# Optimization experiments

Hardware: AMD Instinct MI355X
Metric: run time of the kernel (lower is better)

The kernel has to match this reference:

```python
import jax, jax.numpy as jnp
import numpy as np

B, T, F, H = 64, 128, 188, 16  # batch, time, in_features, feature_embed_dim
N_CONT = F - 11  # features 11.. are continuous (177)


def setup_inputs() -> dict:
    key = jax.random.key(0)
    ks = jax.random.split(key, 14)
    s = 1.0 / np.sqrt(H)  # nn.Linear default init scale
    u = lambda k, shape: jax.random.uniform(k, shape, jnp.float32, -s, s)
    return {
        "x": jax.random.normal(ks[0], (B, T, F * H), jnp.float32),
        # grouped per-feature Linear weights, grouped by output dim
        "W2a": u(ks[1], (4, H, 2)),  "b2a": u(ks[2], (4, 2)),   # features 0-3
        "W3":  u(ks[3], (2, H, 3)),  "b3":  u(ks[4], (2, 3)),   # features 4-5
        "W4":  u(ks[5], (1, H, 4)),  "b4":  u(ks[6], (1, 4)),   # feature 6
        "W6":  u(ks[7], (1, H, 6)),  "b6":  u(ks[8], (1, 6)),   # feature 7
        "W7":  u(ks[9], (3, H, 7)),  "b7":  u(ks[10], (3, 7)),  # features 8-10
        "Wc":  u(ks[11], (N_CONT, H, 2)), "bc": u(ks[12], (N_CONT, 2)),  # features 11..
        "eps": jax.random.normal(ks[13], (B * T, N_CONT), jnp.float32),  # normal-sampling noise
    }


def _cat_argmax(xg, W, b):
    # softmax then argmax == argmax of logits
    logits = jnp.einsum('nfd,fdo->nfo', xg, W) + b
    return jnp.argmax(logits, axis=-1).astype(jnp.float32)


def reference(x, W2a, b2a, W3, b3, W4, b4, W6, b6, W7, b7, Wc, bc, eps):
    xr = x.reshape(B * T, F, H)
    cats = jnp.concatenate([
        _cat_argmax(xr[:, 0:4],  W2a, b2a),
        _cat_argmax(xr[:, 4:6],  W3,  b3),
        _cat_argmax(xr[:, 6:7],  W4,  b4),
        _cat_argmax(xr[:, 7:8],  W6,  b6),
        _cat_argmax(xr[:, 8:11], W7,  b7),
    ], axis=1)  # [N, 11]
    dec = jnp.einsum('nfd,fdo->nfo', xr[:, 11:], Wc) + bc  # [N, 177, 2]
    mean = jnp.tanh(dec[..., 0])
    std = jax.nn.sigmoid(dec[..., 1])
    samp = mean + std * eps  # reparameterized t.normal(mean, std)
    outs = jnp.concatenate([cats, samp], axis=1)  # [N, 188]
    return outs.reshape(B, T, F)
```

## Files before the change

### kernel.cpp

```cpp
#include <hip/hip_runtime.h>
#include <hip/hip_bf16.h>
#include <cmath>

#define NROWS   8192
#define FDIM    188
#define HDIM    16
#define NCONT   177
#define NCAT    11
#define XSTRIDE 3008

__global__ __launch_bounds__(256)
void tab_cont_kernel(const float* __restrict__ x,
                     const float* __restrict__ Wc, const float* __restrict__ bc,
                     const float* __restrict__ eps,
                     float* __restrict__ out)
{
    const int t = blockIdx.x * blockDim.x + threadIdx.x;
    const int n  = t / NCONT;
    const int cf = t - n * NCONT;

    const float4* wp = reinterpret_cast<const float4*>(Wc + cf * 32);
    float4 w0 = wp[0], w1 = wp[1], w2 = wp[2], w3 = wp[3];
    float4 w4 = wp[4], w5 = wp[5], w6 = wp[6], w7 = wp[7];

    const float2 bb = reinterpret_cast<const float2*>(bc)[cf];
    const float  ev = eps[(size_t)n * NCONT + cf];

    const float4* xq = reinterpret_cast<const float4*>(
        x + (size_t)n * XSTRIDE + (size_t)(NCAT + cf) * HDIM);
    float4 a0 = xq[0], a1 = xq[1], a2 = xq[2], a3 = xq[3];

    float m = bb.x, s = bb.y;
    m = fmaf(a0.x, w0.x, m); s = fmaf(a0.x, w0.y, s);
    m = fmaf(a0.y, w0.z, m); s = fmaf(a0.y, w0.w, s);
    m = fmaf(a0.z, w1.x, m); s = fmaf(a0.z, w1.y, s);
    m = fmaf(a0.w, w1.z, m); s = fmaf(a0.w, w1.w, s);
    m = fmaf(a1.x, w2.x, m); s = fmaf(a1.x, w2.y, s);
    m = fmaf(a1.y, w2.z, m); s = fmaf(a1.y, w2.w, s);
    m = fmaf(a1.z, w3.x, m); s = fmaf(a1.z, w3.y, s);
    m = fmaf(a1.w, w3.z, m); s = fmaf(a1.w, w3.w, s);
    m = fmaf(a2.x, w4.x, m); s = fmaf(a2.x, w4.y, s);
    m = fmaf(a2.y, w4.z, m); s = fmaf(a2.y, w4.w, s);
    m = fmaf(a2.z, w5.x, m); s = fmaf(a2.z, w5.y, s);
    m = fmaf(a2.w, w5.z, m); s = fmaf(a2.w, w5.w, s);
    m = fmaf(a3.x, w6.x, m); s = fmaf(a3.x, w6.y, s);
    m = fmaf(a3.y, w6.z, m); s = fmaf(a3.y, w6.w, s);
    m = fmaf(a3.z, w7.x, m); s = fmaf(a3.z, w7.y, s);
    m = fmaf(a3.w, w7.z, m); s = fmaf(a3.w, w7.w, s);

    float mc   = fminf(fmaxf(m, -10.0f), 10.0f);
    float mean = 1.0f - 2.0f / (__expf(2.0f * mc) + 1.0f);
    float stdv = 1.0f / (1.0f + __expf(-s));

    out[(size_t)n * FDIM + NCAT + cf] = fmaf(stdv, ev, mean);
}

__global__ __launch_bounds__(256)
void tab_cat_kernel(const float* __restrict__ x,
                    const float* __restrict__ W2a, const float* __restrict__ b2a,
                    const float* __restrict__ W3,  const float* __restrict__ b3,
                    const float* __restrict__ W4,  const float* __restrict__ b4,
                    const float* __restrict__ W6,  const float* __restrict__ b6,
                    const float* __restrict__ W7,  const float* __restrict__ b7,
                    float* __restrict__ out)
{
    const int t = blockIdx.x * blockDim.x + threadIdx.x;
    if (t >= NROWS * NCAT) return;
    const int n = t / NCAT;
    const int f = t - n * NCAT;

    const float4* xq = reinterpret_cast<const float4*>(
        x + (size_t)n * XSTRIDE + (size_t)f * HDIM);
    float4 a0 = xq[0], a1 = xq[1], a2 = xq[2], a3 = xq[3];
    float xv[16] = { a0.x, a0.y, a0.z, a0.w,
                     a1.x, a1.y, a1.z, a1.w,
                     a2.x, a2.y, a2.z, a2.w,
                     a3.x, a3.y, a3.z, a3.w };

    const float *W, *bb;
    int odim;
    if (f < 4)      { W = W2a + f * HDIM * 2;      bb = b2a + f * 2;      odim = 2; }
    else if (f < 6) { W = W3 + (f - 4) * HDIM * 3; bb = b3 + (f - 4) * 3; odim = 3; }
    else if (f < 7) { W = W4;                      bb = b4;               odim = 4; }
    else if (f < 8) { W = W6;                      bb = b6;               odim = 6; }
    else            { W = W7 + (f - 8) * HDIM * 7; bb = b7 + (f - 8) * 7; odim = 7; }

    float best = -1e30f;
    int   bi   = 0;
    for (int o = 0; o < odim; ++o) {
        float acc = bb[o];
        #pragma unroll
        for (int d = 0; d < 16; ++d) acc = fmaf(xv[d], W[d * odim + o], acc);
        if (acc > best) { best = acc; bi = o; }
    }
    out[(size_t)n * FDIM + f] = (float)bi;
}

extern "C" void kernel_launch(void* const* d_in, const int* in_sizes, int n_in,
                              void* d_out, int out_size, void* d_ws, size_t ws_size,
                              hipStream_t stream) {
    const float* x   = (const float*)d_in[0];
    const float* W2a = (const float*)d_in[1];
    const float* b2a = (const float*)d_in[2];
    const float* W3  = (const float*)d_in[3];
    const float* b3  = (const float*)d_in[4];
    const float* W4  = (const float*)d_in[5];
    const float* b4  = (const float*)d_in[6];
    const float* W6  = (const float*)d_in[7];
    const float* b6  = (const float*)d_in[8];
    const float* W7  = (const float*)d_in[9];
    const float* b7  = (const float*)d_in[10];
    const float* Wc  = (const float*)d_in[11];
    const float* bc  = (const float*)d_in[12];
    const float* eps = (const float*)d_in[13];
    float* out = (float*)d_out;

    hipLaunchKernelGGL(tab_cont_kernel, dim3(NROWS * NCONT / 256), dim3(256), 0, stream,
                       x, Wc, bc, eps, out);
    hipLaunchKernelGGL(tab_cat_kernel, dim3(NROWS * NCAT / 256), dim3(256), 0, stream,
                       x, W2a, b2a, W3, b3, W4, b4, W6, b6, W7, b7, out);
}
```

Before: 190.4 us.

## Fuse continuous and categorical kernels into one launch with LDS-staged weights

Merges the two kernels into a single launch whose blocks branch on blockIdx into continuous or categorical work. Continuous blocks first stage all Wc weights and biases into shared memory in a transposed layout, then read them from LDS instead of global memory. This removes one launch and the gap between kernels. In exchange, every continuous block now pays a cooperative copy of about 23 KB of weights plus a barrier, and the LDS use may limit occupancy.

```diff
diff --git a/kernel.cpp b/kernel.cpp
--- a/kernel.cpp
+++ b/kernel.cpp
@@ -9,91 +9,106 @@
 #define NCAT    11
 #define XSTRIDE 3008
 
-__global__ __launch_bounds__(256)
-void tab_cont_kernel(const float* __restrict__ x,
-                     const float* __restrict__ Wc, const float* __restrict__ bc,
-                     const float* __restrict__ eps,
-                     float* __restrict__ out)
-{
-    const int t = blockIdx.x * blockDim.x + threadIdx.x;
-    const int n  = t / NCONT;
-    const int cf = t - n * NCONT;
+#define CONT_THREADS (NROWS * NCONT)
+#define CONT_BLOCKS  (CONT_THREADS / 256)
+#define CAT_THREADS  (NROWS * NCAT)
+#define CAT_BLOCKS   (CAT_THREADS / 256)
 
-    const float4* wp = reinterpret_cast<const float4*>(Wc + cf * 32);
-    float4 w0 = wp[0], w1 = wp[1], w2 = wp[2], w3 = wp[3];
-    float4 w4 = wp[4], w5 = wp[5], w6 = wp[6], w7 = wp[7];
-
-    const float2 bb = reinterpret_cast<const float2*>(bc)[cf];
-    const float  ev = eps[(size_t)n * NCONT + cf];
-
-    const float4* xq = reinterpret_cast<const float4*>(
-        x + (size_t)n * XSTRIDE + (size_t)(NCAT + cf) * HDIM);
-    float4 a0 = xq[0], a1 = xq[1], a2 = xq[2], a3 = xq[3];
-
-    float m = bb.x, s = bb.y;
-    m = fmaf(a0.x, w0.x, m); s = fmaf(a0.x, w0.y, s);
-    m = fmaf(a0.y, w0.z, m); s = fmaf(a0.y, w0.w, s);
-    m = fmaf(a0.z, w1.x, m); s = fmaf(a0.z, w1.y, s);
-    m = fmaf(a0.w, w1.z, m); s = fmaf(a0.w, w1.w, s);
-    m = fmaf(a1.x, w2.x, m); s = fmaf(a1.x, w2.y, s);
-    m = fmaf(a1.y, w2.z, m); s = fmaf(a1.y, w2.w, s);
-    m = fmaf(a1.z, w3.x, m); s = fmaf(a1.z, w3.y, s);
-    m = fmaf(a1.w, w3.z, m); s = fmaf(a1.w, w3.w, s);
-    m = fmaf(a2.x, w4.x, m); s = fmaf(a2.x, w4.y, s);
-    m = fmaf(a2.y, w4.z, m); s = fmaf(a2.y, w4.w, s);
-    m = fmaf(a2.z, w5.x, m); s = fmaf(a2.z, w5.y, s);
-    m = fmaf(a2.w, w5.z, m); s = fmaf(a2.w, w5.w, s);
-    m = fmaf(a3.x, w6.x, m); s = fmaf(a3.x, w6.y, s);
-    m = fmaf(a3.y, w6.z, m); s = fmaf(a3.y, w6.w, s);
-    m = fmaf(a3.z, w7.x, m); s = fmaf(a3.z, w7.y, s);
-    m = fmaf(a3.w, w7.z, m); s = fmaf(a3.w, w7.w, s);
-
-    float mc   = fminf(fmaxf(m, -10.0f), 10.0f);
-    float mean = 1.0f - 2.0f / (__expf(2.0f * mc) + 1.0f);
-    float stdv = 1.0f / (1.0f + __expf(-s));
-
-    out[(size_t)n * FDIM + NCAT + cf] = fmaf(stdv, ev, mean);
-}
 
 __global__ __launch_bounds__(256)
-void tab_cat_kernel(const float* __restrict__ x,
-                    const float* __restrict__ W2a, const float* __restrict__ b2a,
-                    const float* __restrict__ W3,  const float* __restrict__ b3,
-                    const float* __restrict__ W4,  const float* __restrict__ b4,
-                    const float* __restrict__ W6,  const float* __restrict__ b6,
-                    const float* __restrict__ W7,  const float* __restrict__ b7,
-                    float* __restrict__ out)
+void tab_fused_kernel(const float* __restrict__ x,
+                      const float* __restrict__ W2a, const float* __restrict__ b2a,
+                      const float* __restrict__ W3,  const float* __restrict__ b3,
+                      const float* __restrict__ W4,  const float* __restrict__ b4,
+                      const float* __restrict__ W6,  const float* __restrict__ b6,
+                      const float* __restrict__ W7,  const float* __restrict__ b7,
+                      const float* __restrict__ Wc,  const float* __restrict__ bc,
+                      const float* __restrict__ eps,
+                      float* __restrict__ out)
 {
-    const int t = blockIdx.x * blockDim.x + threadIdx.x;
-    if (t >= NROWS * NCAT) return;
-    const int n = t / NCAT;
-    const int f = t - n * NCAT;
+    __shared__ float4 sW[8 * NCONT];
+    __shared__ float2 sB[NCONT];
 
-    const float4* xq = reinterpret_cast<const float4*>(
-        x + (size_t)n * XSTRIDE + (size_t)f * HDIM);
-    float4 a0 = xq[0], a1 = xq[1], a2 = xq[2], a3 = xq[3];
-    float xv[16] = { a0.x, a0.y, a0.z, a0.w,
-                     a1.x, a1.y, a1.z, a1.w,
-                     a2.x, a2.y, a2.z, a2.w,
-                     a3.x, a3.y, a3.z, a3.w };
+    const int tid = threadIdx.x;
 
-    const float *W, *bb;
-    int odim;
-    if (f < 4)      { W = W2a + f * HDIM * 2;      bb = b2a + f * 2;      odim = 2; }
-    else if (f < 6) { W = W3 + (f - 4) * HDIM * 3; bb = b3 + (f - 4) * 3; odim = 3; }
-    else if (f < 7) { W = W4;                      bb = b4;               odim = 4; }
-    else if (f < 8) { W = W6;                      bb = b6;               odim = 6; }
-    else            { W = W7 + (f - 8) * HDIM * 7; bb = b7 + (f - 8) * 7; odim = 7; }
+    if (blockIdx.x < CONT_BLOCKS) {
+        const float4* wp4 = reinterpret_cast<const float4*>(Wc);
+        for (int i = tid; i < NCONT * 8; i += 256) {
+            int cf = i >> 3, k = i & 7;
+            sW[k * NCONT + cf] = wp4[i];
+        }
+        if (tid < NCONT) sB[tid] = reinterpret_cast<const float2*>(bc)[tid];
+        __syncthreads();
 
-    float best = -1e30f;
-    int   bi   = 0;
-    for (int o = 0; o < odim; ++o) {
-        float acc = bb[o];
-        #pragma unroll
-        for (int d = 0; d < 16; ++d) acc = fmaf(xv[d], W[d * odim + o], acc);
-        if (acc > best) { best = acc; bi = o; }
+        const int t  = blockIdx.x * 256 + tid;
+        const int n  = t / NCONT;
+        const int cf = t - n * NCONT;
+
+        const float4* xq = reinterpret_cast<const float4*>(
+            x + (size_t)n * XSTRIDE + (size_t)(NCAT + cf) * HDIM);
+        float4 a0 = xq[0], a1 = xq[1], a2 = xq[2], a3 = xq[3];
+        const float ev = eps[t];
+
+        float4 w0 = sW[0 * NCONT + cf], w1 = sW[1 * NCONT + cf];
+        float4 w2 = sW[2 * NCONT + cf], w3 = sW[3 * NCONT + cf];
+        float4 w4 = sW[4 * NCONT + cf], w5 = sW[5 * NCONT + cf];
+        float4 w6 = sW[6 * NCONT + cf], w7 = sW[7 * NCONT + cf];
+        float2 bb = sB[cf];
+
+        float m = bb.x, s = bb.y;
+        m = fmaf(a0.x, w0.x, m); s = fmaf(a0.x, w0.y, s);
+        m = fmaf(a0.y, w0.z, m); s = fmaf(a0.y, w0.w, s);
+        m = fmaf(a0.z, w1.x, m); s = fmaf(a0.z, w1.y, s);
+        m = fmaf(a0.w, w1.z, m); s = fmaf(a0.w, w1.w, s);
+        m = fmaf(a1.x, w2.x, m); s = fmaf(a1.x, w2.y, s);
+        m = fmaf(a1.y, w2.z, m); s = fmaf(a1.y, w2.w, s);
+        m = fmaf(a1.z, w3.x, m); s = fmaf(a1.z, w3.y, s);
+        m = fmaf(a1.w, w3.z, m); s = fmaf(a1.w, w3.w, s);
+        m = fmaf(a2.x, w4.x, m); s = fmaf(a2.x, w4.y, s);
+        m = fmaf(a2.y, w4.z, m); s = fmaf(a2.y, w4.w, s);
+        m = fmaf(a2.z, w5.x, m); s = fmaf(a2.z, w5.y, s);
+        m = fmaf(a2.w, w5.z, m); s = fmaf(a2.w, w5.w, s);
+        m = fmaf(a3.x, w6.x, m); s = fmaf(a3.x, w6.y, s);
+        m = fmaf(a3.y, w6.z, m); s = fmaf(a3.y, w6.w, s);
+        m = fmaf(a3.z, w7.x, m); s = fmaf(a3.z, w7.y, s);
+        m = fmaf(a3.w, w7.z, m); s = fmaf(a3.w, w7.w, s);
+
+        float mc   = fminf(fmaxf(m, -10.0f), 10.0f);
+        float mean = 1.0f - 2.0f / (__expf(2.0f * mc) + 1.0f);
+        float stdv = 1.0f / (1.0f + __expf(-s));
+
+        out[(size_t)n * FDIM + NCAT + cf] = fmaf(stdv, ev, mean);
+    } else {
+        const int t = (blockIdx.x - CONT_BLOCKS) * 256 + tid;
+        const int n = t / NCAT;
+        const int f = t - n * NCAT;
+
+        const float4* xq = reinterpret_cast<const float4*>(
+            x + (size_t)n * XSTRIDE + (size_t)f * HDIM);
+        float4 a0 = xq[0], a1 = xq[1], a2 = xq[2], a3 = xq[3];
+        float xv[16] = { a0.x, a0.y, a0.z, a0.w,
+                         a1.x, a1.y, a1.z, a1.w,
+                         a2.x, a2.y, a2.z, a2.w,
+                         a3.x, a3.y, a3.z, a3.w };
+
+        const float *W, *bb;
+        int odim;
+        if (f < 4)      { W = W2a + f * HDIM * 2;      bb = b2a + f * 2;      odim = 2; }
+        else if (f < 6) { W = W3 + (f - 4) * HDIM * 3; bb = b3 + (f - 4) * 3; odim = 3; }
+        else if (f < 7) { W = W4;                      bb = b4;               odim = 4; }
+        else if (f < 8) { W = W6;                      bb = b6;               odim = 6; }
+        else            { W = W7 + (f - 8) * HDIM * 7; bb = b7 + (f - 8) * 7; odim = 7; }
+
+        float best = -1e30f;
+        int   bi   = 0;
+        for (int o = 0; o < odim; ++o) {
+            float acc = bb[o];
+            #pragma unroll
+            for (int d = 0; d < 16; ++d) acc = fmaf(xv[d], W[d * odim + o], acc);
+            if (acc > best) { best = acc; bi = o; }
+        }
+        out[(size_t)n * FDIM + f] = (float)bi;
     }
-    out[(size_t)n * FDIM + f] = (float)bi;
 }
 
 extern "C" void kernel_launch(void* const* d_in, const int* in_sizes, int n_in,
@@ -115,8 +130,6 @@
     const float* eps = (const float*)d_in[13];
     float* out = (float*)d_out;
 
-    hipLaunchKernelGGL(tab_cont_kernel, dim3(NROWS * NCONT / 256), dim3(256), 0, stream,
-                       x, Wc, bc, eps, out);
-    hipLaunchKernelGGL(tab_cat_kernel, dim3(NROWS * NCAT / 256), dim3(256), 0, stream,
-                       x, W2a, b2a, W3, b3, W4, b4, W6, b6, W7, b7, out);
+    hipLaunchKernelGGL(tab_fused_kernel, dim3(CONT_BLOCKS + CAT_BLOCKS), dim3(256), 0, stream,
+                       x, W2a, b2a, W3, b3, W4, b4, W6, b6, W7, b7, Wc, bc, eps, out);
 }
```

Result: no change. 187.2 us (-1.7%).
